# Kernel tuning notes

Measured on AMD Instinct MI355X. Metric: run time of the kernel, lower is better.

Reference implementation:

```python
import jax, jax.numpy as jnp
import numpy as np

T, H, E, I, K = 8192, 2048, 32, 1024, 2


def setup_inputs() -> dict:
    key = jax.random.key(0)
    ks = jax.random.split(key, 6)
    s = 1.0 / np.sqrt(H)
    return {
        "hidden_states": jax.random.normal(ks[0], (T, H), dtype=jnp.float32),
        "router_logits": jax.random.normal(ks[1], (T, E), dtype=jnp.float32),
        "per_expert_scale": jax.random.uniform(ks[2], (E,), dtype=jnp.float32, minval=0.5, maxval=1.5),
        "w_gate": jax.random.normal(ks[3], (E, H, I), dtype=jnp.float32) * s,
        "w_up": jax.random.normal(ks[4], (E, H, I), dtype=jnp.float32) * s,
        "w_down": jax.random.normal(ks[5], (E, I, H), dtype=jnp.float32) * (1.0 / np.sqrt(I)),
        "top_k": K,
    }


def reference(hidden_states, router_logits, per_expert_scale, w_gate, w_up, w_down, top_k):
    num_tokens, hidden_dim = hidden_states.shape
    num_experts = w_gate.shape[0]
    # Gemma4 routing: top-k over raw logits, softmax over the k logits
    # (== full softmax renormalized over top-k), scaled per expert.
    topk_logits, topk_ids = jax.lax.top_k(router_logits, top_k)  # [T,K]
    topk_weights = jax.nn.softmax(topk_logits, axis=-1) * per_expert_scale[topk_ids]
    # Dense combine matrix [T,E]: weight for expert e if selected, else 0.
    cw = jnp.zeros((num_tokens, num_experts), hidden_states.dtype)
    cw = cw.at[jnp.arange(num_tokens)[:, None], topk_ids].add(
        topk_weights.astype(hidden_states.dtype))
    # Gated GELU MLP per expert, weighted accumulate (scan keeps memory small).
    def body(acc, ws):
        wg, wu, wd, c = ws  # c: [T] combine weight for this expert
        h = jax.nn.gelu(hidden_states @ wg, approximate=False) * (hidden_states @ wu)
        return acc + c[:, None] * (h @ wd), None
    acc0 = jnp.zeros_like(hidden_states)
    out, _ = jax.lax.scan(body, acc0, (w_gate, w_up, w_down, cw.T))
    return out
```

## Files before the change

### kernel.cpp

```cpp
#include <hip/hip_runtime.h>

#define T_TOK 8192
#define HDIM  2048
#define NEXP  32
#define IDIM  1024

#define BM 128
#define BN 128
#define BK 64
#define CAP (T_TOK*2 + NEXP*BM)
#define MAX_RT (CAP/BM)
#define CVB 8192
#define NTB 2048

typedef __attribute__((ext_vector_type(8))) short bh8;
typedef __attribute__((ext_vector_type(4))) float f4;

__device__ __forceinline__ unsigned short f2bf(float f) {
    unsigned u = __builtin_bit_cast(unsigned, f);
    u += 0x7FFFu + ((u >> 16) & 1u);
    return (unsigned short)(u >> 16);
}

__device__ __forceinline__ int swz(int row, int kb) {
    return row * 128 + (kb ^ ((row & 7) << 4));
}

__device__ __forceinline__ void gload16(const void* g, void* l) {
    __builtin_amdgcn_global_load_lds(
        (const __attribute__((address_space(1))) unsigned int*)g,
        (__attribute__((address_space(3))) unsigned int*)l,
        16, 0, 0);
}


__device__ __forceinline__ void top2(const float* __restrict__ l,
                                     int& b1, float& v1, int& b2, float& v2) {
    v1 = -1e30f; b1 = 0;
#pragma unroll
    for (int e = 0; e < NEXP; ++e) { float v = l[e]; if (v > v1) { v1 = v; b1 = e; } }
    v2 = -1e30f; b2 = 0;
#pragma unroll
    for (int e = 0; e < NEXP; ++e) { if (e == b1) continue; float v = l[e]; if (v > v2) { v2 = v; b2 = e; } }
}

__global__ void route_count_kernel(const float* __restrict__ logits, int* __restrict__ counts) {
    int t = blockIdx.x * blockDim.x + threadIdx.x;
    if (t >= T_TOK) return;
    int b1, b2; float v1, v2;
    top2(logits + (size_t)t * NEXP, b1, v1, b2, v2);
    atomicAdd(&counts[b1], 1);
    atomicAdd(&counts[b2], 1);
}

__global__ void offsets_kernel(const int* __restrict__ counts, int* __restrict__ offs) {
    if (threadIdx.x == 0) {
        int o = 0;
        for (int e = 0; e < NEXP; ++e) { offs[e] = o; o += (counts[e] + BM - 1) & ~(BM - 1); }
        offs[NEXP] = o;
    }
}

__global__ void route_scatter_kernel(const float* __restrict__ logits,
                                     const float* __restrict__ scale,
                                     const int* __restrict__ offs,
                                     int* __restrict__ cursor,
                                     int* __restrict__ row_tok,
                                     float* __restrict__ row_w) {
    int t = blockIdx.x * blockDim.x + threadIdx.x;
    if (t >= T_TOK) return;
    int b1, b2; float v1, v2;
    top2(logits + (size_t)t * NEXP, b1, v1, b2, v2);
    float e2 = expf(v2 - v1);
    float inv = 1.0f / (1.0f + e2);
    float w1 = scale[b1] * inv;
    float w2 = scale[b2] * e2 * inv;
    int p1 = offs[b1] + atomicAdd(&cursor[b1], 1);
    row_tok[p1] = t; row_w[p1] = w1;
    int p2 = offs[b2] + atomicAdd(&cursor[b2], 1);
    row_tok[p2] = t; row_w[p2] = w2;
}


__device__ __forceinline__ void half_dma(const float* __restrict__ in, int K, int N,
                                         int e, int k0, int n0, char* ldsH, int t) {
    const char* src = (const char*)(in + (size_t)e * K * N + (size_t)k0 * N + n0);
    int w = t >> 6;
#pragma unroll
    for (int i = 0; i < 8; ++i) {
        int c = i * 256 + t;
        int k = c >> 5;
        int cc = (c & 31) ^ (((k >> 3) & 7) << 2);
        gload16(src + (size_t)k * N * 4 + (size_t)cc * 16, ldsH + i * 4096 + w * 1024);
    }
}

__device__ __forceinline__ void half_store(unsigned short* __restrict__ out, int K, int N,
                                           int e, int k0, int n0, const char* ldsH, int t) {
    unsigned short* dst = out + (size_t)e * K * N + (size_t)n0 * K + k0;
    int kg = t & 7, nb = t >> 3;
#pragma unroll
    for (int p = 0; p < 4; ++p) {
        int n = nb + 32 * p;
        bh8 v;
#pragma unroll
        for (int j = 0; j < 8; ++j) {
            int kl = 8 * kg + j;
            int boff = kl * 512 + ((((n >> 2) ^ ((kg & 7) << 2)) << 4)) + (n & 3) * 4;
            v[j] = (short)f2bf(*(const float*)(ldsH + boff));
        }
        *(bh8*)(dst + (size_t)n * K + 8 * kg) = v;
    }
}

__device__ __forceinline__ void tile_params(int g,
                                            const float* wg, const float* wu, const float* wd,
                                            unsigned short* wgT, unsigned short* wuT, unsigned short* wdT,
                                            const float*& in, unsigned short*& out,
                                            int& K, int& N, int& e, int& k0, int& n0) {
    int mat = g >> 12;
    int loc = g & 4095;
    e = loc >> 7;
    int tl = loc & 127;
    if (mat == 2) { in = wd; out = wdT; K = IDIM; N = HDIM; k0 = (tl >> 4) << 7; n0 = (tl & 15) << 7; }
    else if (mat == 1) { in = wu; out = wuT; K = HDIM; N = IDIM; k0 = (tl >> 3) << 7; n0 = (tl & 7) << 7; }
    else { in = wg; out = wgT; K = HDIM; N = IDIM; k0 = (tl >> 3) << 7; n0 = (tl & 7) << 7; }
}

__global__ void prep_all(const float* __restrict__ hs, unsigned short* __restrict__ hsb,
                         const float* __restrict__ wg, unsigned short* __restrict__ wgT,
                         const float* __restrict__ wu, unsigned short* __restrict__ wuT,
                         const float* __restrict__ wd, unsigned short* __restrict__ wdT,
                         int nTiles) {
    __shared__ float lds4[16384];
    int b = blockIdx.x;
    int t = threadIdx.x;
    if (b < CVB) {
        size_t i = ((size_t)b * 256 + t) * 8;
        float4 a = *(const float4*)(hs + i);
        float4 c = *(const float4*)(hs + i + 4);
        bh8 v;
        v[0] = (short)f2bf(a.x); v[1] = (short)f2bf(a.y);
        v[2] = (short)f2bf(a.z); v[3] = (short)f2bf(a.w);
        v[4] = (short)f2bf(c.x); v[5] = (short)f2bf(c.y);
        v[6] = (short)f2bf(c.z); v[7] = (short)f2bf(c.w);
        *(bh8*)(hsb + i) = v;
        return;
    }
    int tb = b - CVB;
    char* L0 = (char*)lds4;
    char* L1 = L0 + 32768;
    int nq = nTiles / NTB;

    {
        const float* in; unsigned short* o; int K, N, e, k0, n0;
        tile_params(tb, wg, wu, wd, wgT, wuT, wdT, in, o, K, N, e, k0, n0);
        half_dma(in, K, N, e, k0, n0, L0, t);
    }
    __syncthreads();

    int cur = 0;
    for (int q = 0; q < nq; ++q) {
        const float* in; unsigned short* o; int K, N, e, k0, n0;
        tile_params(tb + q * NTB, wg, wu, wd, wgT, wuT, wdT, in, o, K, N, e, k0, n0);
#pragma unroll
        for (int hh = 0; hh < 2; ++hh) {
            int nq2 = q, nh = hh + 1;
            if (nh == 2) { nq2 = q + 1; nh = 0; }
            if (nq2 < nq) {
                const float* in2; unsigned short* o2; int K2, N2, e2, k02, n02;
                tile_params(tb + nq2 * NTB, wg, wu, wd, wgT, wuT, wdT, in2, o2, K2, N2, e2, k02, n02);
                half_dma(in2, K2, N2, e2, k02 + nh * 64, n02, cur ? L0 : L1, t);
            }
            half_store(o, K, N, e, k0 + hh * 64, n0, cur ? L1 : L0, t);
            __syncthreads();
            cur ^= 1;
        }
    }
}

__global__ void transpose_wd_kernel(const float* __restrict__ wd, unsigned short* __restrict__ wdT) {
    __shared__ float lds4[16384];
    int tb = blockIdx.x, t = threadIdx.x;
    char* L0 = (char*)lds4;
    char* L1 = L0 + 32768;
    auto prm = [&](int g, int& e, int& k0, int& n0) {
        e = g >> 7; int tl = g & 127;
        k0 = (tl >> 4) << 7; n0 = (tl & 15) << 7;
    };
    int e, k0, n0;
    prm(tb, e, k0, n0);
    half_dma(wd, IDIM, HDIM, e, k0, n0, L0, t);
    __syncthreads();
    int cur = 0;
    for (int q = 0; q < 2; ++q) {
        int eq, kq, nq0;
        prm(tb + q * NTB, eq, kq, nq0);
#pragma unroll
        for (int hh = 0; hh < 2; ++hh) {
            int q2 = q, nh = hh + 1;
            if (nh == 2) { q2 = q + 1; nh = 0; }
            if (q2 < 2) {
                int e2, k2, n2;
                prm(tb + q2 * NTB, e2, k2, n2);
                half_dma(wd, IDIM, HDIM, e2, k2 + nh * 64, n2, cur ? L0 : L1, t);
            }
            half_store(wdT, IDIM, HDIM, eq, kq + hh * 64, nq0, cur ? L1 : L0, t);
            __syncthreads();
            cur ^= 1;
        }
    }
}

__launch_bounds__(256, 2)
__global__ void gemm1n_kernel(const unsigned short* __restrict__ hsb,
                              const unsigned short* __restrict__ wgT,
                              const unsigned short* __restrict__ wuT,
                              const int* __restrict__ offs,
                              const int* __restrict__ row_tok,
                              unsigned short* __restrict__ act) {
    __shared__ char lds[49152];
    char* Xb = lds;
    char* Gb = lds + 16384;
    char* Ub = lds + 32768;

    int rt = blockIdx.x >> 3;
    int nt = blockIdx.x & 7;
    int total = offs[NEXP];
    if (rt * BM >= total) return;
    int e = 0;
    while (offs[e + 1] <= rt * BM) e++;

    int tid = threadIdx.x, l = tid & 63, wv = tid >> 6;
    int wm = wv >> 1, wn = wv & 1;

    unsigned srcChunk = ((l & 7) * 16) ^ ((l >> 3) << 4);

    unsigned xoff[4], goff[4];
#pragma unroll
    for (int i = 0; i < 4; ++i) {
        int r = i * 32 + wv * 8 + (l >> 3);
        int tok = row_tok[rt * BM + r];
        if (tok < 0) tok = 0;
        xoff[i] = (unsigned)tok * (HDIM * 2) + srcChunk;
        unsigned wrow = (unsigned)e * IDIM + nt * BN + r;
        goff[i] = wrow * (HDIM * 2) + srcChunk;
    }

    f4 accG[4][4], accU[4][4];
#pragma unroll
    for (int mi = 0; mi < 4; ++mi)
#pragma unroll
        for (int ni = 0; ni < 4; ++ni) { accG[mi][ni] = (f4)0.0f; accU[mi][ni] = (f4)0.0f; }

    const char* hsc = (const char*)hsb;
    const char* wgc = (const char*)wgT;
    const char* wuc = (const char*)wuT;

    for (int kt = 0; kt < HDIM / BK; ++kt) {
        unsigned kby = kt * 128;
#pragma unroll
        for (int i = 0; i < 4; ++i)
            gload16(hsc + (size_t)xoff[i] + kby, Xb + i * 4096 + wv * 1024);
#pragma unroll
        for (int i = 0; i < 4; ++i)
            gload16(wgc + (size_t)goff[i] + kby, Gb + i * 4096 + wv * 1024);
#pragma unroll
        for (int i = 0; i < 4; ++i)
            gload16(wuc + (size_t)goff[i] + kby, Ub + i * 4096 + wv * 1024);
        __syncthreads();

#pragma unroll
        for (int ks = 0; ks < 2; ++ks) {
            int kb = ks * 64 + ((l >> 4) << 4);
            bh8 a[4], g[4], u[4];
#pragma unroll
            for (int mi = 0; mi < 4; ++mi)
                a[mi] = *(const bh8*)(Xb + swz(wm * 64 + mi * 16 + (l & 15), kb));
#pragma unroll
            for (int ni = 0; ni < 4; ++ni) {
                int nr = wn * 64 + ni * 16 + (l & 15);
                g[ni] = *(const bh8*)(Gb + swz(nr, kb));
                u[ni] = *(const bh8*)(Ub + swz(nr, kb));
            }
#pragma unroll
            for (int mi = 0; mi < 4; ++mi)
#pragma unroll
                for (int ni = 0; ni < 4; ++ni) {
                    accG[mi][ni] = __builtin_amdgcn_mfma_f32_16x16x32_bf16(a[mi], g[ni], accG[mi][ni], 0, 0, 0);
                    accU[mi][ni] = __builtin_amdgcn_mfma_f32_16x16x32_bf16(a[mi], u[ni], accU[mi][ni], 0, 0, 0);
                }
        }
        __syncthreads();
    }

    char* actc = (char*)act;
#pragma unroll
    for (int mi = 0; mi < 4; ++mi) {
#pragma unroll
        for (int i = 0; i < 4; ++i) {
            int r = rt * BM + wm * 64 + mi * 16 + ((l >> 4) << 2) + i;
            size_t rowbase = (size_t)r * (IDIM * 2);
            int rs = (r & 7) << 4;
#pragma unroll
            for (int ni = 0; ni < 4; ++ni) {
                int col = nt * BN + wn * 64 + ni * 16 + (l & 15);
                float gv = accG[mi][ni][i], uv = accU[mi][ni][i];
                float gl = 0.5f * gv * (1.0f + erff(gv * 0.70710678118654752f));
                *(unsigned short*)(actc + rowbase + ((col * 2) ^ rs)) = f2bf(gl * uv);
            }
        }
    }
}

__launch_bounds__(256, 2)
__global__ void gemm2n_kernel(const unsigned short* __restrict__ act,
                              const unsigned short* __restrict__ wdT,
                              const int* __restrict__ offs,
                              const int* __restrict__ row_tok,
                              const float* __restrict__ row_w,
                              float* __restrict__ out) {
    __shared__ char lds[49152];
    char* Xb = lds;
    char* Db = lds + 16384;

    int rt = blockIdx.x >> 3;
    int nt = blockIdx.x & 7;
    int total = offs[NEXP];
    if (rt * BM >= total) return;
    int e = 0;
    while (offs[e + 1] <= rt * BM) e++;

    int tid = threadIdx.x, l = tid & 63, wv = tid >> 6;
    int wm = wv >> 1, wn = wv & 1;

    unsigned srcChunk = ((l & 7) * 16) ^ ((l >> 3) << 4);

    unsigned aoff[4];
#pragma unroll
    for (int i = 0; i < 4; ++i) {
        int r = i * 32 + wv * 8 + (l >> 3);
        aoff[i] = (unsigned)(rt * BM + r) * (IDIM * 2) + (l & 7) * 16;
    }
    unsigned doff[8];
#pragma unroll
    for (int i = 0; i < 8; ++i) {
        int r = i * 32 + wv * 8 + (l >> 3);
        doff[i] = ((unsigned)e * HDIM + nt * 256 + r) * (IDIM * 2) + srcChunk;
    }

    f4 acc[4][8];
#pragma unroll
    for (int mi = 0; mi < 4; ++mi)
#pragma unroll
        for (int ni = 0; ni < 8; ++ni) acc[mi][ni] = (f4)0.0f;

    const char* actc = (const char*)act;
    const char* wdc = (const char*)wdT;

    for (int kt = 0; kt < IDIM / BK; ++kt) {
        unsigned kby = kt * 128;
#pragma unroll
        for (int i = 0; i < 4; ++i)
            gload16(actc + (size_t)aoff[i] + kby, Xb + i * 4096 + wv * 1024);
#pragma unroll
        for (int i = 0; i < 8; ++i)
            gload16(wdc + (size_t)doff[i] + kby, Db + i * 4096 + wv * 1024);
        __syncthreads();

#pragma unroll
        for (int ks = 0; ks < 2; ++ks) {
            int kb = ks * 64 + ((l >> 4) << 4);
            bh8 a[4], b[8];
#pragma unroll
            for (int mi = 0; mi < 4; ++mi)
                a[mi] = *(const bh8*)(Xb + swz(wm * 64 + mi * 16 + (l & 15), kb));
#pragma unroll
            for (int ni = 0; ni < 8; ++ni)
                b[ni] = *(const bh8*)(Db + swz(wn * 128 + ni * 16 + (l & 15), kb));
#pragma unroll
            for (int mi = 0; mi < 4; ++mi)
#pragma unroll
                for (int ni = 0; ni < 8; ++ni)
                    acc[mi][ni] = __builtin_amdgcn_mfma_f32_16x16x32_bf16(a[mi], b[ni], acc[mi][ni], 0, 0, 0);
        }
        __syncthreads();
    }

#pragma unroll
    for (int mi = 0; mi < 4; ++mi) {
#pragma unroll
        for (int i = 0; i < 4; ++i) {
            int r = rt * BM + wm * 64 + mi * 16 + ((l >> 4) << 2) + i;
            int tok = row_tok[r];
            if (tok < 0) continue;
            float w = row_w[r];
            float* op = out + (size_t)tok * HDIM + nt * 256 + wn * 128 + (l & 15);
#pragma unroll
            for (int ni = 0; ni < 8; ++ni)
                atomicAdd(op + ni * 16, acc[mi][ni][i] * w);
        }
    }
}


extern "C" void kernel_launch(void* const* d_in, const int* in_sizes, int n_in,
                              void* d_out, int out_size, void* d_ws, size_t ws_size,
                              hipStream_t stream) {
    const float* hs     = (const float*)d_in[0];
    const float* logits = (const float*)d_in[1];
    const float* scale  = (const float*)d_in[2];
    const float* wg     = (const float*)d_in[3];
    const float* wu     = (const float*)d_in[4];
    const float* wd     = (const float*)d_in[5];
    float* out = (float*)d_out;

    char* ws = (char*)d_ws;
    int*   counts  = (int*)ws;
    int*   cursor  = counts + 32;
    int*   offs    = cursor + 32;
    int*   row_tok = (int*)(ws + 512);
    float* row_w   = (float*)(ws + 512 + (size_t)CAP * 4);

    size_t base = 512 + (size_t)CAP * 8;
    size_t actB = (size_t)CAP * IDIM * 2;
    size_t hsB  = (size_t)T_TOK * HDIM * 2;
    size_t wTB  = (size_t)NEXP * IDIM * HDIM * 2;

    unsigned short* act = (unsigned short*)(ws + base);
    unsigned short* hsb = (unsigned short*)(ws + base + actB);
    unsigned short* wgT = (unsigned short*)(ws + base + actB + hsB);
    unsigned short* wuT = (unsigned short*)(ws + base + actB + hsB + wTB);
    unsigned short* wdT = (unsigned short*)(ws + base + actB + hsB + 2 * wTB);

    size_t need3 = base + actB + hsB + 3 * wTB;
    bool full = (ws_size >= need3);

    hipMemsetAsync(counts, 0, 512, stream);
    hipMemsetAsync(row_tok, 0xFF, (size_t)CAP * 4, stream);
    hipMemsetAsync(out, 0, (size_t)out_size * sizeof(float), stream);

    route_count_kernel<<<T_TOK / 256, 256, 0, stream>>>(logits, counts);
    offsets_kernel<<<1, 64, 0, stream>>>(counts, offs);
    route_scatter_kernel<<<T_TOK / 256, 256, 0, stream>>>(logits, scale, offs, cursor, row_tok, row_w);

    if (full) {
        prep_all<<<CVB + NTB, 256, 0, stream>>>(hs, hsb, wg, wgT, wu, wuT, wd, wdT, 12288);
        gemm1n_kernel<<<MAX_RT * 8, 256, 0, stream>>>(hsb, wgT, wuT, offs, row_tok, act);
        gemm2n_kernel<<<MAX_RT * 8, 256, 0, stream>>>(act, wdT, offs, row_tok, row_w, out);
    } else {
        prep_all<<<CVB + NTB, 256, 0, stream>>>(hs, hsb, wg, wgT, wu, wuT, wd, wdT, 8192);
        gemm1n_kernel<<<MAX_RT * 8, 256, 0, stream>>>(hsb, wgT, wuT, offs, row_tok, act);
        transpose_wd_kernel<<<NTB, 256, 0, stream>>>(wd, wgT);
        gemm2n_kernel<<<MAX_RT * 8, 256, 0, stream>>>(act, wgT, offs, row_tok, row_w, out);
    }
}
```

Baseline: 718.9 us.

## Add 256x256-tile 8-wave MoE GEMM path with split gate/up passes

Adds a templated 512-thread GEMM kernel with 256x256 output tiles, double-buffered LDS with phased loads and barriers, and priority hints around MFMA blocks. It pads expert segments to 256 rows and runs the up projection, then the gate projection fused with GELU times up, then the down projection with weighted atomic accumulation. The new path is used when the workspace is large enough for an extra up-projection buffer; otherwise it falls back to the old kernels. The goal is higher MFMA utilisation through larger tiles. In exchange it adds padding waste, an extra activation round trip through memory, and uses one block per CU.

```diff
diff --git a/kernel.cpp b/kernel.cpp
--- a/kernel.cpp
+++ b/kernel.cpp
@@ -7,9 +7,10 @@
 
 #define BM 128
 #define BN 128
-#define BK 64
-#define CAP (T_TOK*2 + NEXP*BM)
-#define MAX_RT (CAP/BM)
+#define CAPO (T_TOK*2 + NEXP*128)
+#define CAPN (T_TOK*2 + NEXP*256)
+#define MAX_RT (CAPO/128)
+#define RT256 (CAPN/256)
 #define CVB 8192
 #define NTB 2048
 
@@ -21,18 +22,18 @@
     u += 0x7FFFu + ((u >> 16) & 1u);
     return (unsigned short)(u >> 16);
 }
-
+__device__ __forceinline__ float bf2f(unsigned short s) {
+    return __builtin_bit_cast(float, (unsigned)s << 16);
+}
 __device__ __forceinline__ int swz(int row, int kb) {
     return row * 128 + (kb ^ ((row & 7) << 4));
 }
-
 __device__ __forceinline__ void gload16(const void* g, void* l) {
     __builtin_amdgcn_global_load_lds(
         (const __attribute__((address_space(1))) unsigned int*)g,
         (__attribute__((address_space(3))) unsigned int*)l,
         16, 0, 0);
 }
-
 
 __device__ __forceinline__ void top2(const float* __restrict__ l,
                                      int& b1, float& v1, int& b2, float& v2) {
@@ -53,10 +54,10 @@
     atomicAdd(&counts[b2], 1);
 }
 
-__global__ void offsets_kernel(const int* __restrict__ counts, int* __restrict__ offs) {
+__global__ void offsets_kernel(const int* __restrict__ counts, int* __restrict__ offs, int align) {
     if (threadIdx.x == 0) {
         int o = 0;
-        for (int e = 0; e < NEXP; ++e) { offs[e] = o; o += (counts[e] + BM - 1) & ~(BM - 1); }
+        for (int e = 0; e < NEXP; ++e) { offs[e] = o; o += (counts[e] + align - 1) & ~(align - 1); }
         offs[NEXP] = o;
     }
 }
@@ -81,7 +82,6 @@
     row_tok[p2] = t; row_w[p2] = w2;
 }
 
-
 __device__ __forceinline__ void half_dma(const float* __restrict__ in, int K, int N,
                                          int e, int k0, int n0, char* ldsH, int t) {
     const char* src = (const char*)(in + (size_t)e * K * N + (size_t)k0 * N + n0);
@@ -94,7 +94,6 @@
         gload16(src + (size_t)k * N * 4 + (size_t)cc * 16, ldsH + i * 4096 + w * 1024);
     }
 }
-
 __device__ __forceinline__ void half_store(unsigned short* __restrict__ out, int K, int N,
                                            int e, int k0, int n0, const char* ldsH, int t) {
     unsigned short* dst = out + (size_t)e * K * N + (size_t)n0 * K + k0;
@@ -112,7 +111,6 @@
         *(bh8*)(dst + (size_t)n * K + 8 * kg) = v;
     }
 }
-
 __device__ __forceinline__ void tile_params(int g,
                                             const float* wg, const float* wu, const float* wd,
                                             unsigned short* wgT, unsigned short* wuT, unsigned short* wdT,
@@ -126,7 +124,6 @@
     else if (mat == 1) { in = wu; out = wuT; K = HDIM; N = IDIM; k0 = (tl >> 3) << 7; n0 = (tl & 7) << 7; }
     else { in = wg; out = wgT; K = HDIM; N = IDIM; k0 = (tl >> 3) << 7; n0 = (tl & 7) << 7; }
 }
-
 __global__ void prep_all(const float* __restrict__ hs, unsigned short* __restrict__ hsb,
                          const float* __restrict__ wg, unsigned short* __restrict__ wgT,
                          const float* __restrict__ wu, unsigned short* __restrict__ wuT,
@@ -151,14 +148,12 @@
     char* L0 = (char*)lds4;
     char* L1 = L0 + 32768;
     int nq = nTiles / NTB;
-
     {
         const float* in; unsigned short* o; int K, N, e, k0, n0;
         tile_params(tb, wg, wu, wd, wgT, wuT, wdT, in, o, K, N, e, k0, n0);
         half_dma(in, K, N, e, k0, n0, L0, t);
     }
     __syncthreads();
-
     int cur = 0;
     for (int q = 0; q < nq; ++q) {
         const float* in; unsigned short* o; int K, N, e, k0, n0;
@@ -178,7 +173,6 @@
         }
     }
 }
-
 __global__ void transpose_wd_kernel(const float* __restrict__ wd, unsigned short* __restrict__ wdT) {
     __shared__ float lds4[16384];
     int tb = blockIdx.x, t = threadIdx.x;
@@ -212,6 +206,144 @@
     }
 }
 
+template<int MODE>
+__launch_bounds__(512, 1)
+__global__ void gemm8p(const unsigned short* __restrict__ Abase,
+                       const unsigned short* __restrict__ Bw,
+                       const int* __restrict__ offs,
+                       const int* __restrict__ row_tok,
+                       const float* __restrict__ row_w,
+                       const unsigned short* __restrict__ uin,
+                       unsigned short* __restrict__ outb,
+                       float* __restrict__ outf) {
+    constexpr int K   = (MODE == 2) ? IDIM : HDIM;
+    constexpr int NT  = K / 64;
+    constexpr int N0  = (MODE == 2) ? HDIM : IDIM;
+    constexpr int NTL = N0 / 256;
+
+    __shared__ char lds[131072];
+
+    int bid = blockIdx.x;
+    int rt = bid / NTL, nt = bid % NTL;
+    if (rt * 256 >= offs[NEXP]) return;
+    int e = 0;
+    while (offs[e + 1] <= rt * 256) e++;
+
+    int t = threadIdx.x, l = t & 63, w = t >> 6;
+    int wm = w >> 2, wn = w & 3;
+
+    unsigned srcx = ((l & 7) * 16) ^ ((l >> 3) << 4);
+    unsigned aoff[4];
+#pragma unroll
+    for (int j = 0; j < 4; ++j) {
+        int r = rt * 256 + j * 64 + (t >> 3);
+        if (MODE == 2) {
+            aoff[j] = (unsigned)r * (K * 2) + (l & 7) * 16;
+        } else {
+            int tok = row_tok[r];
+            if (tok < 0) tok = 0;
+            aoff[j] = (unsigned)tok * (K * 2) + srcx;
+        }
+    }
+    unsigned boff[4];
+#pragma unroll
+    for (int j = 0; j < 4; ++j) {
+        unsigned br = (unsigned)e * N0 + nt * 256 + j * 64 + (t >> 3);
+        boff[j] = br * (K * 2) + srcx;
+    }
+    const char* Ac = (const char*)Abase;
+    const char* Bc = (const char*)Bw;
+
+    f4 acc[8][4];
+#pragma unroll
+    for (int mi = 0; mi < 8; ++mi)
+#pragma unroll
+        for (int ni = 0; ni < 4; ++ni) acc[mi][ni] = (f4)0.0f;
+
+#define STG(H, NB, KT1) {                                                    \
+    size_t kby_ = (size_t)(KT1) * 128;                                       \
+    _Pragma("unroll")                                                        \
+    for (int i_ = 0; i_ < 2; ++i_) {                                         \
+        const char* s_ = ((H) < 2) ? (Ac + (size_t)aoff[(H) * 2 + i_] + kby_)\
+                                   : (Bc + (size_t)boff[((H) - 2) * 2 + i_] + kby_); \
+        gload16(s_, lds + (NB) * 65536 + (H) * 16384 + i_ * 8192 + w * 1024);\
+    } }
+
+    STG(0, 0, 0) STG(1, 0, 0) STG(2, 0, 0) STG(3, 0, 0)
+    __syncthreads();
+
+    int kb0 = (l >> 4) << 4;
+
+#define PH(P) {                                                              \
+    STG(P, nb, ktn)                                                          \
+    if ((P) == 0) asm volatile("s_waitcnt vmcnt(2)" ::: "memory");           \
+    __builtin_amdgcn_s_barrier();                                            \
+    const char* Ab_ = lds + cb * 65536 + wm * 16384;                         \
+    const char* Bb_ = lds + cb * 65536 + 32768 + (wn >> 1) * 16384;          \
+    int kb_ = ((P) >> 1) * 64 + kb0;                                         \
+    bh8 aA[4], bB[4];                                                        \
+    _Pragma("unroll")                                                        \
+    for (int j_ = 0; j_ < 4; ++j_)                                           \
+        aA[j_] = *(const bh8*)(Ab_ + swz(((P & 1) * 4 + j_) * 16 + (l & 15), kb_)); \
+    _Pragma("unroll")                                                        \
+    for (int n_ = 0; n_ < 4; ++n_)                                           \
+        bB[n_] = *(const bh8*)(Bb_ + swz((wn & 1) * 64 + n_ * 16 + (l & 15), kb_)); \
+    asm volatile("s_waitcnt lgkmcnt(0)" ::: "memory");                       \
+    __builtin_amdgcn_sched_barrier(0);                                       \
+    __builtin_amdgcn_s_setprio(1);                                           \
+    _Pragma("unroll")                                                        \
+    for (int j_ = 0; j_ < 4; ++j_)                                           \
+        _Pragma("unroll")                                                    \
+        for (int n_ = 0; n_ < 4; ++n_)                                       \
+            acc[(P & 1) * 4 + j_][n_] = __builtin_amdgcn_mfma_f32_16x16x32_bf16( \
+                aA[j_], bB[n_], acc[(P & 1) * 4 + j_][n_], 0, 0, 0);         \
+    __builtin_amdgcn_s_setprio(0);                                           \
+    __builtin_amdgcn_s_barrier();                                            \
+}
+
+    for (int kt = 0; kt < NT; ++kt) {
+        int cb = kt & 1;
+        int nb = cb ^ 1;
+        int ktn = (kt + 1 < NT) ? kt + 1 : 0;
+        PH(0) PH(1) PH(2) PH(3)
+    }
+#undef PH
+#undef STG
+
+#pragma unroll
+    for (int mi = 0; mi < 8; ++mi) {
+#pragma unroll
+        for (int i = 0; i < 4; ++i) {
+            int gr = rt * 256 + wm * 128 + mi * 16 + ((l >> 4) << 2) + i;
+            if (MODE == 2) {
+                int tok = row_tok[gr];
+                if (tok < 0) continue;
+                float wgt = row_w[gr];
+                float* op = outf + (size_t)tok * HDIM + nt * 256 + wn * 64 + (l & 15);
+#pragma unroll
+                for (int ni = 0; ni < 4; ++ni)
+                    atomicAdd(op + ni * 16, acc[mi][ni][i] * wgt);
+            } else {
+                size_t rowbase = (size_t)gr * (N0 * 2);
+                int rs = (gr & 7) << 4;
+#pragma unroll
+                for (int ni = 0; ni < 4; ++ni) {
+                    int col = nt * 256 + wn * 64 + ni * 16 + (l & 15);
+                    size_t addr = rowbase + (size_t)((col * 2) ^ rs);
+                    if (MODE == 0) {
+                        *(unsigned short*)((char*)outb + addr) = f2bf(acc[mi][ni][i]);
+                    } else {
+                        float uu = bf2f(*(const unsigned short*)((const char*)uin + addr));
+                        float g = acc[mi][ni][i];
+                        float gl = 0.5f * g * (1.0f + erff(g * 0.70710678118654752f));
+                        *(unsigned short*)((char*)outb + addr) = f2bf(gl * uu);
+                    }
+                }
+            }
+        }
+    }
+}
+
 __launch_bounds__(256, 2)
 __global__ void gemm1n_kernel(const unsigned short* __restrict__ hsb,
                               const unsigned short* __restrict__ wgT,
@@ -233,7 +365,6 @@
 
     int tid = threadIdx.x, l = tid & 63, wv = tid >> 6;
     int wm = wv >> 1, wn = wv & 1;
-
     unsigned srcChunk = ((l & 7) * 16) ^ ((l >> 3) << 4);
 
     unsigned xoff[4], goff[4];
@@ -257,7 +388,7 @@
     const char* wgc = (const char*)wgT;
     const char* wuc = (const char*)wuT;
 
-    for (int kt = 0; kt < HDIM / BK; ++kt) {
+    for (int kt = 0; kt < HDIM / 64; ++kt) {
         unsigned kby = kt * 128;
 #pragma unroll
         for (int i = 0; i < 4; ++i)
@@ -333,7 +464,6 @@
 
     int tid = threadIdx.x, l = tid & 63, wv = tid >> 6;
     int wm = wv >> 1, wn = wv & 1;
-
     unsigned srcChunk = ((l & 7) * 16) ^ ((l >> 3) << 4);
 
     unsigned aoff[4];
@@ -358,7 +488,7 @@
     const char* actc = (const char*)act;
     const char* wdc = (const char*)wdT;
 
-    for (int kt = 0; kt < IDIM / BK; ++kt) {
+    for (int kt = 0; kt < IDIM / 64; ++kt) {
         unsigned kby = kt * 128;
 #pragma unroll
         for (int i = 0; i < 4; ++i)
@@ -420,36 +550,58 @@
     int*   cursor  = counts + 32;
     int*   offs    = cursor + 32;
     int*   row_tok = (int*)(ws + 512);
-    float* row_w   = (float*)(ws + 512 + (size_t)CAP * 4);
-
-    size_t base = 512 + (size_t)CAP * 8;
-    size_t actB = (size_t)CAP * IDIM * 2;
-    size_t hsB  = (size_t)T_TOK * HDIM * 2;
-    size_t wTB  = (size_t)NEXP * IDIM * HDIM * 2;
-
-    unsigned short* act = (unsigned short*)(ws + base);
-    unsigned short* hsb = (unsigned short*)(ws + base + actB);
-    unsigned short* wgT = (unsigned short*)(ws + base + actB + hsB);
-    unsigned short* wuT = (unsigned short*)(ws + base + actB + hsB + wTB);
-    unsigned short* wdT = (unsigned short*)(ws + base + actB + hsB + 2 * wTB);
-
-    size_t need3 = base + actB + hsB + 3 * wTB;
-    bool full = (ws_size >= need3);
+    float* row_w   = (float*)(ws + 512 + (size_t)CAPN * 4);
+
+    size_t base  = 512 + (size_t)CAPN * 8;
+    size_t actBN = (size_t)CAPN * IDIM * 2;
+    size_t actBO = (size_t)CAPO * IDIM * 2;
+    size_t hsB   = (size_t)T_TOK * HDIM * 2;
+    size_t wTB   = (size_t)NEXP * IDIM * HDIM * 2;
+
+    size_t needFull = base + 2 * actBN + hsB + 3 * wTB;
+    size_t needMid  = base + actBO + hsB + 3 * wTB;
 
     hipMemsetAsync(counts, 0, 512, stream);
-    hipMemsetAsync(row_tok, 0xFF, (size_t)CAP * 4, stream);
+    hipMemsetAsync(row_tok, 0xFF, (size_t)CAPN * 4, stream);
     hipMemsetAsync(out, 0, (size_t)out_size * sizeof(float), stream);
 
     route_count_kernel<<<T_TOK / 256, 256, 0, stream>>>(logits, counts);
-    offsets_kernel<<<1, 64, 0, stream>>>(counts, offs);
-    route_scatter_kernel<<<T_TOK / 256, 256, 0, stream>>>(logits, scale, offs, cursor, row_tok, row_w);
-
-    if (full) {
+
+    if (ws_size >= needFull) {
+        unsigned short* act  = (unsigned short*)(ws + base);
+        unsigned short* ubuf = (unsigned short*)(ws + base + actBN);
+        unsigned short* hsb  = (unsigned short*)(ws + base + 2 * actBN);
+        unsigned short* wgT  = (unsigned short*)(ws + base + 2 * actBN + hsB);
+        unsigned short* wuT  = (unsigned short*)(ws + base + 2 * actBN + hsB + wTB);
+        unsigned short* wdT  = (unsigned short*)(ws + base + 2 * actBN + hsB + 2 * wTB);
+
+        offsets_kernel<<<1, 64, 0, stream>>>(counts, offs, 256);
+        route_scatter_kernel<<<T_TOK / 256, 256, 0, stream>>>(logits, scale, offs, cursor, row_tok, row_w);
+        prep_all<<<CVB + NTB, 256, 0, stream>>>(hs, hsb, wg, wgT, wu, wuT, wd, wdT, 12288);
+        gemm8p<0><<<RT256 * 4, 512, 0, stream>>>(hsb, wuT, offs, row_tok, row_w, nullptr, ubuf, nullptr);
+        gemm8p<1><<<RT256 * 4, 512, 0, stream>>>(hsb, wgT, offs, row_tok, row_w, ubuf, act, nullptr);
+        gemm8p<2><<<RT256 * 8, 512, 0, stream>>>(act, wdT, offs, row_tok, row_w, nullptr, nullptr, out);
+    } else if (ws_size >= needMid) {
+        unsigned short* act = (unsigned short*)(ws + base);
+        unsigned short* hsb = (unsigned short*)(ws + base + actBO);
+        unsigned short* wgT = (unsigned short*)(ws + base + actBO + hsB);
+        unsigned short* wuT = (unsigned short*)(ws + base + actBO + hsB + wTB);
+        unsigned short* wdT = (unsigned short*)(ws + base + actBO + hsB + 2 * wTB);
+
+        offsets_kernel<<<1, 64, 0, stream>>>(counts, offs, 128);
+        route_scatter_kernel<<<T_TOK / 256, 256, 0, stream>>>(logits, scale, offs, cursor, row_tok, row_w);
         prep_all<<<CVB + NTB, 256, 0, stream>>>(hs, hsb, wg, wgT, wu, wuT, wd, wdT, 12288);
         gemm1n_kernel<<<MAX_RT * 8, 256, 0, stream>>>(hsb, wgT, wuT, offs, row_tok, act);
         gemm2n_kernel<<<MAX_RT * 8, 256, 0, stream>>>(act, wdT, offs, row_tok, row_w, out);
     } else {
-        prep_all<<<CVB + NTB, 256, 0, stream>>>(hs, hsb, wg, wgT, wu, wuT, wd, wdT, 8192);
+        unsigned short* act = (unsigned short*)(ws + base);
+        unsigned short* hsb = (unsigned short*)(ws + base + actBO);
+        unsigned short* wgT = (unsigned short*)(ws + base + actBO + hsB);
+        unsigned short* wuT = (unsigned short*)(ws + base + actBO + hsB + wTB);
+
+        offsets_kernel<<<1, 64, 0, stream>>>(counts, offs, 128);
+        route_scatter_kernel<<<T_TOK / 256, 256, 0, stream>>>(logits, scale, offs, cursor, row_tok, row_w);
+        prep_all<<<CVB + NTB, 256, 0, stream>>>(hs, hsb, wg, wgT, wu, wuT, nullptr, nullptr, 8192);
         gemm1n_kernel<<<MAX_RT * 8, 256, 0, stream>>>(hsb, wgT, wuT, offs, row_tok, act);
         transpose_wd_kernel<<<NTB, 256, 0, stream>>>(wd, wgT);
         gemm2n_kernel<<<MAX_RT * 8, 256, 0, stream>>>(act, wgT, offs, row_tok, row_w, out);
```

New measurement: 847.4 us. 17.9% more time.

## Widen MoE GEMM blocks to 8 waves and add XCD-aware block swizzle

Applied to the files above, without the earlier changes.

Both expert GEMM kernels now run with 512 threads (8 waves in a 2x4 grid) per 128-row tile instead of 4 waves, so each wave holds half as many accumulators. Launch bounds go from 256,2 to 512,4, aiming at more resident waves to hide latency. Block IDs are remapped with an XCD swizzle so neighbouring tiles, which share expert weights, land on the same XCD's L2. The tradeoff is more LDS-load work per MFMA and tighter register limits, which could cause spills.

```diff
diff --git a/kernel.cpp b/kernel.cpp
--- a/kernel.cpp
+++ b/kernel.cpp
@@ -6,10 +6,9 @@
 #define IDIM  1024
 
 #define BM 128
-#define BN 128
-#define BK 64
-#define CAP (T_TOK*2 + NEXP*BM)
-#define MAX_RT (CAP/BM)
+#define CAP (T_TOK*2 + NEXP*128)
+#define MAX_RT (CAP/128)
+#define G1N (MAX_RT*8)
 #define CVB 8192
 #define NTB 2048
 
@@ -21,18 +20,18 @@
     u += 0x7FFFu + ((u >> 16) & 1u);
     return (unsigned short)(u >> 16);
 }
-
 __device__ __forceinline__ int swz(int row, int kb) {
     return row * 128 + (kb ^ ((row & 7) << 4));
 }
-
 __device__ __forceinline__ void gload16(const void* g, void* l) {
     __builtin_amdgcn_global_load_lds(
         (const __attribute__((address_space(1))) unsigned int*)g,
         (__attribute__((address_space(3))) unsigned int*)l,
         16, 0, 0);
 }
-
+__device__ __forceinline__ int xcd_swz(int b, int nwg) {
+    return (b & 7) * (nwg >> 3) + (b >> 3);
+}
 
 __device__ __forceinline__ void top2(const float* __restrict__ l,
                                      int& b1, float& v1, int& b2, float& v2) {
@@ -56,7 +55,7 @@
 __global__ void offsets_kernel(const int* __restrict__ counts, int* __restrict__ offs) {
     if (threadIdx.x == 0) {
         int o = 0;
-        for (int e = 0; e < NEXP; ++e) { offs[e] = o; o += (counts[e] + BM - 1) & ~(BM - 1); }
+        for (int e = 0; e < NEXP; ++e) { offs[e] = o; o += (counts[e] + 127) & ~127; }
         offs[NEXP] = o;
     }
 }
@@ -81,7 +80,6 @@
     row_tok[p2] = t; row_w[p2] = w2;
 }
 
-
 __device__ __forceinline__ void half_dma(const float* __restrict__ in, int K, int N,
                                          int e, int k0, int n0, char* ldsH, int t) {
     const char* src = (const char*)(in + (size_t)e * K * N + (size_t)k0 * N + n0);
@@ -94,7 +92,6 @@
         gload16(src + (size_t)k * N * 4 + (size_t)cc * 16, ldsH + i * 4096 + w * 1024);
     }
 }
-
 __device__ __forceinline__ void half_store(unsigned short* __restrict__ out, int K, int N,
                                            int e, int k0, int n0, const char* ldsH, int t) {
     unsigned short* dst = out + (size_t)e * K * N + (size_t)n0 * K + k0;
@@ -112,7 +109,6 @@
         *(bh8*)(dst + (size_t)n * K + 8 * kg) = v;
     }
 }
-
 __device__ __forceinline__ void tile_params(int g,
                                             const float* wg, const float* wu, const float* wd,
                                             unsigned short* wgT, unsigned short* wuT, unsigned short* wdT,
@@ -126,7 +122,6 @@
     else if (mat == 1) { in = wu; out = wuT; K = HDIM; N = IDIM; k0 = (tl >> 3) << 7; n0 = (tl & 7) << 7; }
     else { in = wg; out = wgT; K = HDIM; N = IDIM; k0 = (tl >> 3) << 7; n0 = (tl & 7) << 7; }
 }
-
 __global__ void prep_all(const float* __restrict__ hs, unsigned short* __restrict__ hsb,
                          const float* __restrict__ wg, unsigned short* __restrict__ wgT,
                          const float* __restrict__ wu, unsigned short* __restrict__ wuT,
@@ -151,14 +146,12 @@
     char* L0 = (char*)lds4;
     char* L1 = L0 + 32768;
     int nq = nTiles / NTB;
-
     {
         const float* in; unsigned short* o; int K, N, e, k0, n0;
         tile_params(tb, wg, wu, wd, wgT, wuT, wdT, in, o, K, N, e, k0, n0);
         half_dma(in, K, N, e, k0, n0, L0, t);
     }
     __syncthreads();
-
     int cur = 0;
     for (int q = 0; q < nq; ++q) {
         const float* in; unsigned short* o; int K, N, e, k0, n0;
@@ -178,7 +171,6 @@
         }
     }
 }
-
 __global__ void transpose_wd_kernel(const float* __restrict__ wd, unsigned short* __restrict__ wdT) {
     __shared__ float lds4[16384];
     int tb = blockIdx.x, t = threadIdx.x;
@@ -212,8 +204,8 @@
     }
 }
 
-__launch_bounds__(256, 2)
-__global__ void gemm1n_kernel(const unsigned short* __restrict__ hsb,
+__launch_bounds__(512, 4)
+__global__ void gemm1w_kernel(const unsigned short* __restrict__ hsb,
                               const unsigned short* __restrict__ wgT,
                               const unsigned short* __restrict__ wuT,
                               const int* __restrict__ offs,
@@ -224,69 +216,65 @@
     char* Gb = lds + 16384;
     char* Ub = lds + 32768;
 
-    int rt = blockIdx.x >> 3;
-    int nt = blockIdx.x & 7;
-    int total = offs[NEXP];
-    if (rt * BM >= total) return;
+    int gid = xcd_swz(blockIdx.x, G1N);
+    int rt = gid >> 3;
+    int nt = gid & 7;
+    if (rt * BM >= offs[NEXP]) return;
     int e = 0;
     while (offs[e + 1] <= rt * BM) e++;
 
-    int tid = threadIdx.x, l = tid & 63, wv = tid >> 6;
-    int wm = wv >> 1, wn = wv & 1;
-
-    unsigned srcChunk = ((l & 7) * 16) ^ ((l >> 3) << 4);
-
-    unsigned xoff[4], goff[4];
-#pragma unroll
-    for (int i = 0; i < 4; ++i) {
-        int r = i * 32 + wv * 8 + (l >> 3);
+    int t = threadIdx.x, l = t & 63, w = t >> 6;
+    int wm = w >> 2, wn = w & 3;
+
+    unsigned srcx = ((l & 7) * 16) ^ ((l >> 3) << 4);
+
+    unsigned xoff[2], goff[2];
+#pragma unroll
+    for (int i = 0; i < 2; ++i) {
+        int r = (w * 2 + i) * 8 + (l >> 3);
         int tok = row_tok[rt * BM + r];
         if (tok < 0) tok = 0;
-        xoff[i] = (unsigned)tok * (HDIM * 2) + srcChunk;
-        unsigned wrow = (unsigned)e * IDIM + nt * BN + r;
-        goff[i] = wrow * (HDIM * 2) + srcChunk;
-    }
-
-    f4 accG[4][4], accU[4][4];
-#pragma unroll
-    for (int mi = 0; mi < 4; ++mi)
-#pragma unroll
-        for (int ni = 0; ni < 4; ++ni) { accG[mi][ni] = (f4)0.0f; accU[mi][ni] = (f4)0.0f; }
-
+        xoff[i] = (unsigned)tok * (HDIM * 2) + srcx;
+        goff[i] = ((unsigned)e * IDIM + nt * 128 + r) * (HDIM * 2) + srcx;
+    }
     const char* hsc = (const char*)hsb;
     const char* wgc = (const char*)wgT;
     const char* wuc = (const char*)wuT;
 
-    for (int kt = 0; kt < HDIM / BK; ++kt) {
+    f4 accG[4][2], accU[4][2];
+#pragma unroll
+    for (int mi = 0; mi < 4; ++mi)
+#pragma unroll
+        for (int ni = 0; ni < 2; ++ni) { accG[mi][ni] = (f4)0.0f; accU[mi][ni] = (f4)0.0f; }
+
+    for (int kt = 0; kt < HDIM / 64; ++kt) {
         unsigned kby = kt * 128;
 #pragma unroll
-        for (int i = 0; i < 4; ++i)
-            gload16(hsc + (size_t)xoff[i] + kby, Xb + i * 4096 + wv * 1024);
-#pragma unroll
-        for (int i = 0; i < 4; ++i)
-            gload16(wgc + (size_t)goff[i] + kby, Gb + i * 4096 + wv * 1024);
-#pragma unroll
-        for (int i = 0; i < 4; ++i)
-            gload16(wuc + (size_t)goff[i] + kby, Ub + i * 4096 + wv * 1024);
+        for (int i = 0; i < 2; ++i) {
+            int co = (w * 2 + i) * 1024;
+            gload16(hsc + (size_t)xoff[i] + kby, Xb + co);
+            gload16(wgc + (size_t)goff[i] + kby, Gb + co);
+            gload16(wuc + (size_t)goff[i] + kby, Ub + co);
+        }
         __syncthreads();
 
 #pragma unroll
         for (int ks = 0; ks < 2; ++ks) {
             int kb = ks * 64 + ((l >> 4) << 4);
-            bh8 a[4], g[4], u[4];
+            bh8 a[4], g[2], u[2];
 #pragma unroll
             for (int mi = 0; mi < 4; ++mi)
                 a[mi] = *(const bh8*)(Xb + swz(wm * 64 + mi * 16 + (l & 15), kb));
 #pragma unroll
-            for (int ni = 0; ni < 4; ++ni) {
-                int nr = wn * 64 + ni * 16 + (l & 15);
+            for (int ni = 0; ni < 2; ++ni) {
+                int nr = wn * 32 + ni * 16 + (l & 15);
                 g[ni] = *(const bh8*)(Gb + swz(nr, kb));
                 u[ni] = *(const bh8*)(Ub + swz(nr, kb));
             }
 #pragma unroll
             for (int mi = 0; mi < 4; ++mi)
 #pragma unroll
-                for (int ni = 0; ni < 4; ++ni) {
+                for (int ni = 0; ni < 2; ++ni) {
                     accG[mi][ni] = __builtin_amdgcn_mfma_f32_16x16x32_bf16(a[mi], g[ni], accG[mi][ni], 0, 0, 0);
                     accU[mi][ni] = __builtin_amdgcn_mfma_f32_16x16x32_bf16(a[mi], u[ni], accU[mi][ni], 0, 0, 0);
                 }
@@ -303,8 +291,8 @@
             size_t rowbase = (size_t)r * (IDIM * 2);
             int rs = (r & 7) << 4;
 #pragma unroll
-            for (int ni = 0; ni < 4; ++ni) {
-                int col = nt * BN + wn * 64 + ni * 16 + (l & 15);
+            for (int ni = 0; ni < 2; ++ni) {
+                int col = nt * 128 + wn * 32 + ni * 16 + (l & 15);
                 float gv = accG[mi][ni][i], uv = accU[mi][ni][i];
                 float gl = 0.5f * gv * (1.0f + erff(gv * 0.70710678118654752f));
                 *(unsigned short*)(actc + rowbase + ((col * 2) ^ rs)) = f2bf(gl * uv);
@@ -313,8 +301,8 @@
     }
 }
 
-__launch_bounds__(256, 2)
-__global__ void gemm2n_kernel(const unsigned short* __restrict__ act,
+__launch_bounds__(512, 4)
+__global__ void gemm2w_kernel(const unsigned short* __restrict__ act,
                               const unsigned short* __restrict__ wdT,
                               const int* __restrict__ offs,
                               const int* __restrict__ row_tok,
@@ -324,64 +312,63 @@
     char* Xb = lds;
     char* Db = lds + 16384;
 
-    int rt = blockIdx.x >> 3;
-    int nt = blockIdx.x & 7;
-    int total = offs[NEXP];
-    if (rt * BM >= total) return;
+    int gid = xcd_swz(blockIdx.x, G1N);
+    int rt = gid >> 3;
+    int nt = gid & 7;
+    if (rt * BM >= offs[NEXP]) return;
     int e = 0;
     while (offs[e + 1] <= rt * BM) e++;
 
-    int tid = threadIdx.x, l = tid & 63, wv = tid >> 6;
-    int wm = wv >> 1, wn = wv & 1;
-
-    unsigned srcChunk = ((l & 7) * 16) ^ ((l >> 3) << 4);
-
-    unsigned aoff[4];
+    int t = threadIdx.x, l = t & 63, w = t >> 6;
+    int wm = w >> 2, wn = w & 3;
+
+    unsigned srcx = ((l & 7) * 16) ^ ((l >> 3) << 4);
+
+    unsigned aoff[2];
+#pragma unroll
+    for (int i = 0; i < 2; ++i) {
+        int r = (w * 2 + i) * 8 + (l >> 3);
+        aoff[i] = (unsigned)(rt * BM + r) * (IDIM * 2) + (l & 7) * 16;
+    }
+    unsigned doff[4];
 #pragma unroll
     for (int i = 0; i < 4; ++i) {
-        int r = i * 32 + wv * 8 + (l >> 3);
-        aoff[i] = (unsigned)(rt * BM + r) * (IDIM * 2) + (l & 7) * 16;
-    }
-    unsigned doff[8];
-#pragma unroll
-    for (int i = 0; i < 8; ++i) {
-        int r = i * 32 + wv * 8 + (l >> 3);
-        doff[i] = ((unsigned)e * HDIM + nt * 256 + r) * (IDIM * 2) + srcChunk;
-    }
-
-    f4 acc[4][8];
-#pragma unroll
-    for (int mi = 0; mi < 4; ++mi)
-#pragma unroll
-        for (int ni = 0; ni < 8; ++ni) acc[mi][ni] = (f4)0.0f;
-
+        int r = (w * 4 + i) * 8 + (l >> 3);
+        doff[i] = ((unsigned)e * HDIM + nt * 256 + r) * (IDIM * 2) + srcx;
+    }
     const char* actc = (const char*)act;
     const char* wdc = (const char*)wdT;
 
-    for (int kt = 0; kt < IDIM / BK; ++kt) {
+    f4 acc[4][4];
+#pragma unroll
+    for (int mi = 0; mi < 4; ++mi)
+#pragma unroll
+        for (int ni = 0; ni < 4; ++ni) acc[mi][ni] = (f4)0.0f;
+
+    for (int kt = 0; kt < IDIM / 64; ++kt) {
         unsigned kby = kt * 128;
 #pragma unroll
+        for (int i = 0; i < 2; ++i)
+            gload16(actc + (size_t)aoff[i] + kby, Xb + (w * 2 + i) * 1024);
+#pragma unroll
         for (int i = 0; i < 4; ++i)
-            gload16(actc + (size_t)aoff[i] + kby, Xb + i * 4096 + wv * 1024);
-#pragma unroll
-        for (int i = 0; i < 8; ++i)
-            gload16(wdc + (size_t)doff[i] + kby, Db + i * 4096 + wv * 1024);
+            gload16(wdc + (size_t)doff[i] + kby, Db + (w * 4 + i) * 1024);
         __syncthreads();
 
 #pragma unroll
         for (int ks = 0; ks < 2; ++ks) {
             int kb = ks * 64 + ((l >> 4) << 4);
-            bh8 a[4], b[8];
+            bh8 a[4], b[4];
 #pragma unroll
             for (int mi = 0; mi < 4; ++mi)
                 a[mi] = *(const bh8*)(Xb + swz(wm * 64 + mi * 16 + (l & 15), kb));
 #pragma unroll
-            for (int ni = 0; ni < 8; ++ni)
-                b[ni] = *(const bh8*)(Db + swz(wn * 128 + ni * 16 + (l & 15), kb));
+            for (int ni = 0; ni < 4; ++ni)
+                b[ni] = *(const bh8*)(Db + swz(wn * 64 + ni * 16 + (l & 15), kb));
 #pragma unroll
             for (int mi = 0; mi < 4; ++mi)
 #pragma unroll
-                for (int ni = 0; ni < 8; ++ni)
+                for (int ni = 0; ni < 4; ++ni)
                     acc[mi][ni] = __builtin_amdgcn_mfma_f32_16x16x32_bf16(a[mi], b[ni], acc[mi][ni], 0, 0, 0);
         }
         __syncthreads();
@@ -394,11 +381,11 @@
             int r = rt * BM + wm * 64 + mi * 16 + ((l >> 4) << 2) + i;
             int tok = row_tok[r];
             if (tok < 0) continue;
-            float w = row_w[r];
-            float* op = out + (size_t)tok * HDIM + nt * 256 + wn * 128 + (l & 15);
-#pragma unroll
-            for (int ni = 0; ni < 8; ++ni)
-                atomicAdd(op + ni * 16, acc[mi][ni][i] * w);
+            float wgt = row_w[r];
+            float* op = out + (size_t)tok * HDIM + nt * 256 + wn * 64 + (l & 15);
+#pragma unroll
+            for (int ni = 0; ni < 4; ++ni)
+                atomicAdd(op + ni * 16, acc[mi][ni][i] * wgt);
         }
     }
 }
@@ -446,12 +433,12 @@
 
     if (full) {
         prep_all<<<CVB + NTB, 256, 0, stream>>>(hs, hsb, wg, wgT, wu, wuT, wd, wdT, 12288);
-        gemm1n_kernel<<<MAX_RT * 8, 256, 0, stream>>>(hsb, wgT, wuT, offs, row_tok, act);
-        gemm2n_kernel<<<MAX_RT * 8, 256, 0, stream>>>(act, wdT, offs, row_tok, row_w, out);
+        gemm1w_kernel<<<G1N, 512, 0, stream>>>(hsb, wgT, wuT, offs, row_tok, act);
+        gemm2w_kernel<<<G1N, 512, 0, stream>>>(act, wdT, offs, row_tok, row_w, out);
     } else {
-        prep_all<<<CVB + NTB, 256, 0, stream>>>(hs, hsb, wg, wgT, wu, wuT, wd, wdT, 8192);
-        gemm1n_kernel<<<MAX_RT * 8, 256, 0, stream>>>(hsb, wgT, wuT, offs, row_tok, act);
+        prep_all<<<CVB + NTB, 256, 0, stream>>>(hs, hsb, wg, wgT, wu, wuT, nullptr, nullptr, 8192);
+        gemm1w_kernel<<<G1N, 512, 0, stream>>>(hsb, wgT, wuT, offs, row_tok, act);
         transpose_wd_kernel<<<NTB, 256, 0, stream>>>(wd, wgT);
-        gemm2n_kernel<<<MAX_RT * 8, 256, 0, stream>>>(act, wgT, offs, row_tok, row_w, out);
-    }
-}
+        gemm2w_kernel<<<G1N, 512, 0, stream>>>(act, wgT, offs, row_tok, row_w, out);
+    }
+}
```

Result: slower. 875.5 us (+21.8%).
